# Kernel optimization log

Measured on AMD Instinct MI355X. Metric: run time of the kernel, lower is better.

Reference implementation:

```python
import jax, jax.numpy as jnp
import numpy as np

EPS = 1e-5
K = 16  # neighbors

def bn(x, g, b):
    # BatchNorm in training mode: stats over all axes except the last (channel)
    ax = tuple(range(x.ndim - 1))
    m = x.mean(ax, keepdims=True)
    v = x.var(ax, keepdims=True)
    return g * (x - m) * jax.lax.rsqrt(v + EPS) + b

def setup_inputs() -> dict:
    key = jax.random.key(0)
    ks = jax.random.split(key, 12)
    B, N, M, C, D = 2, 16384, 4096, 32, 64
    H = D // 2
    p = lambda k, s: jax.random.normal(k, s, dtype=jnp.float32) * 0.1
    inp = {}
    inp["xyz"] = jax.random.normal(ks[0], (B, N, 3), dtype=jnp.float32)
    inp["feats"] = jax.random.normal(ks[1], (B, C, N), dtype=jnp.float32)
    inp["sample_idx"] = jax.random.randint(ks[2], (B, M), 0, N, dtype=jnp.int32)
    # RelativePosEncoder mlp: Conv2d(10, H, 1) + BN
    inp["W_pos"] = p(ks[3], (10, H)); inp["b_pos"] = jnp.zeros(H); inp["g_pos"] = jnp.ones(H); inp["be_pos"] = jnp.zeros(H)
    # feature_mlp: Conv2d(C, H, 1) + BN
    inp["W_feat"] = p(ks[4], (C, H)); inp["b_feat"] = jnp.zeros(H); inp["g_feat"] = jnp.ones(H); inp["be_feat"] = jnp.zeros(H)
    # attention score mlp: Conv2d(D, D, 1, bias=False)
    inp["W_score"] = p(ks[5], (D, D))
    # out_mlp: Conv1d(D, D, 1, bias=False) + BN
    inp["W_out"] = p(ks[6], (D, D)); inp["g_out"] = jnp.ones(D); inp["be_out"] = jnp.zeros(D)
    # LFA shortcut: Conv1d(C, D, 1, bias=False) + BN
    inp["W_sc1"] = p(ks[7], (C, D)); inp["g_sc1"] = jnp.ones(D); inp["be_sc1"] = jnp.zeros(D)
    # unit shortcut: Conv1d(C, D, 1, bias=False) + BN
    inp["W_sc2"] = p(ks[8], (C, D)); inp["g_sc2"] = jnp.ones(D); inp["be_sc2"] = jnp.zeros(D)
    return inp

def reference(xyz, feats, sample_idx,
              W_pos, b_pos, g_pos, be_pos,
              W_feat, b_feat, g_feat, be_feat,
              W_score,
              W_out, g_out, be_out,
              W_sc1, g_sc1, be_sc1,
              W_sc2, g_sc2, be_sc2):
    B, C, N = feats.shape
    featsT = jnp.transpose(feats, (0, 2, 1))                    # [B,N,C]
    xyz_ds = jnp.take_along_axis(xyz, sample_idx[:, :, None], axis=1)  # [B,M,3]
    # KNN: squared distances are monotone in cdist -> same topk indices
    d2 = jnp.sum((xyz_ds[:, :, None, :] - xyz[:, None, :, :]) ** 2, axis=-1)  # [B,M,N]
    _, knn_idx = jax.lax.top_k(-d2, K)                           # [B,M,K]
    gather = jax.vmap(lambda pts, idx: pts[idx])
    neigh_xyz = gather(xyz, knn_idx)                             # [B,M,K,3]
    neigh_feats = gather(featsT, knn_idx)                        # [B,M,K,C]
    center_feats = jnp.take_along_axis(featsT, sample_idx[:, :, None], axis=1)  # [B,M,C]
    # relative position encoding
    center = jnp.broadcast_to(xyz_ds[:, :, None, :], neigh_xyz.shape)
    rel = xyz_ds[:, :, None, :] - neigh_xyz                      # [B,M,K,3]
    dist = jnp.linalg.norm(rel, axis=-1, keepdims=True)          # [B,M,K,1]
    posf = jnp.concatenate([center, neigh_xyz, rel, dist], axis=-1)  # [B,M,K,10]
    pos_feats = jax.nn.relu(bn(posf @ W_pos + b_pos, g_pos, be_pos))       # [B,M,K,H]
    feat_feats = jax.nn.relu(bn(neigh_feats @ W_feat + b_feat, g_feat, be_feat))  # [B,M,K,H]
    combined = jnp.concatenate([feat_feats, pos_feats], axis=-1)  # [B,M,K,D]
    # attention pooling: softmax over the K (neighbor) axis
    scores = jax.nn.softmax(combined @ W_score, axis=2)
    pooled = jnp.sum(scores * combined, axis=2)                  # [B,M,D]
    out = jax.nn.relu(bn(pooled @ W_out, g_out, be_out))         # [B,M,D]
    sc1 = bn(jnp.mean(neigh_feats, axis=2) @ W_sc1, g_sc1, be_sc1)
    f_lfa = out + sc1
    f_sc = bn(center_feats @ W_sc2, g_sc2, be_sc2)
    y = jax.nn.relu(f_lfa + f_sc)                                # [B,M,D]
    return xyz_ds, jnp.transpose(y, (0, 2, 1)), sample_idx
```

## Files before the change

kernel.cpp:

```cpp
#include <hip/hip_runtime.h>
#include <math.h>

#define BB 2
#define NN 16384
#define MM 4096
#define C_IN 32
#define D_DIM 64
#define H_DIM 32
#define KNB 16
#define EPSV 1e-5f
#define FLT_BIG 3.0e38f
#define CAPK 128
#define NSPL 4
#define SPTS (NN / NSPL)

#define SPOS_SUM 0
#define SPOS_SQ 32
#define SFEAT_SUM 64
#define SFEAT_SQ 96
#define SSC1_SUM 128
#define SSC1_SQ 192
#define SSC2_SUM 256
#define SSC2_SQ 320
#define SOUT_SUM 384
#define SOUT_SQ 448
#define STATS_LEN 512
#define PA_W 384
#define PB_W 128
#define NBLK (BB * MM / 4)

__device__ __forceinline__ int clampi_r17(int v, int lo, int hi) {
    return v < lo ? lo : (v > hi ? hi : v);
}

__global__ __launch_bounds__(256) void prep_r17(const float* __restrict__ feats,
                                                const float* __restrict__ xyz,
                                                const int* __restrict__ sample_idx,
                                                float* __restrict__ featsT,
                                                float* __restrict__ xyz4,
                                                float* __restrict__ stats,
                                                float* __restrict__ out) {
    __shared__ float tile[C_IN][65];
    const int tid = threadIdx.x;
    const int b = blockIdx.x >> 8;
    const int n0 = (blockIdx.x & 255) * 64;
#pragma unroll
    for (int it = 0; it < 8; ++it) {
        int c = (tid >> 6) + 4 * it;
        int n = tid & 63;
        tile[c][n] = feats[((size_t)b * C_IN + c) * NN + n0 + n];
    }
    int e = blockIdx.x * 256 + tid;
    if (e < STATS_LEN) stats[e] = 0.f;
    if (e < BB * NN) {
        float x = xyz[e * 3 + 0], y = xyz[e * 3 + 1], z = xyz[e * 3 + 2];
        xyz4[e * 4 + 0] = x;
        xyz4[e * 4 + 1] = y;
        xyz4[e * 4 + 2] = z;
        xyz4[e * 4 + 3] = x * x + y * y + z * z;
    }
    if (e < BB * MM) {
        int bb2 = e >> 12;
        int sidx = clampi_r17(sample_idx[e], 0, NN - 1);
        const float* p = xyz + (size_t)(bb2 * NN + sidx) * 3;
        out[e * 3 + 0] = p[0];
        out[e * 3 + 1] = p[1];
        out[e * 3 + 2] = p[2];
        out[BB * MM * 3 + BB * D_DIM * MM + e] = (float)sample_idx[e];
    }
    __syncthreads();
#pragma unroll
    for (int it = 0; it < 8; ++it) {
        int c = tid & 31;
        int nn = (tid >> 5) + 8 * it;
        featsT[((size_t)b * NN + n0 + nn) * C_IN + c] = tile[c][nn];
    }
}

__device__ void knn_fullsplit_r17(const float* __restrict__ base4, int n0,
                                  float m2x, float m2y, float m2z, int lane,
                                  float* __restrict__ outd, int* __restrict__ outi) {
    float d2v[KNB]; int iv[KNB];
#pragma unroll
    for (int i = 0; i < KNB; i++) { d2v[i] = FLT_BIG; iv[i] = 0x7FFFFFFF; }
    float curmax = FLT_BIG; int amax = 0;
    for (int t = 0; t < SPTS / 64; ++t) {
        int n = n0 + lane + t * 64;
        const float4 p = *reinterpret_cast<const float4*>(base4 + (size_t)n * 4);
        float d2 = fmaf(p.x, m2x, p.w);
        d2 = fmaf(p.y, m2y, d2);
        d2 = fmaf(p.z, m2z, d2);
        if (d2 < curmax) {
#pragma unroll
            for (int i = 0; i < KNB; i++)
                if (i == amax) { d2v[i] = d2; iv[i] = n; }
            curmax = d2v[0]; amax = 0;
#pragma unroll
            for (int i = 1; i < KNB; i++)
                if (d2v[i] > curmax) { curmax = d2v[i]; amax = i; }
        }
    }
#pragma unroll
    for (int i = 0; i < KNB; i++) {
#pragma unroll
        for (int j = 0; j < KNB - 1; j++) {
            bool sw = (d2v[j] > d2v[j + 1]) ||
                      (d2v[j] == d2v[j + 1] && iv[j] > iv[j + 1]);
            if (sw) {
                float td = d2v[j]; d2v[j] = d2v[j + 1]; d2v[j + 1] = td;
                int   ti = iv[j];  iv[j]  = iv[j + 1];  iv[j + 1]  = ti;
            }
        }
    }
    float myd = FLT_BIG; int myidx = 0x7FFFFFFF;
#pragma unroll 1
    for (int r = 0; r < KNB; r++) {
        float cv = d2v[0]; int cid = iv[0]; int ml = lane;
#pragma unroll
        for (int off = 32; off > 0; off >>= 1) {
            float ov = __shfl_xor(cv, off);
            int   oid = __shfl_xor(cid, off);
            int   ol = __shfl_xor(ml, off);
            bool take = (ov < cv) || (ov == cv && oid < cid);
            cv = take ? ov : cv; cid = take ? oid : cid; ml = take ? ol : ml;
        }
        if (lane == r) { myd = cv; myidx = cid; }
        if (lane == ml) {
#pragma unroll
            for (int i = 0; i < KNB - 1; i++) { d2v[i] = d2v[i + 1]; iv[i] = iv[i + 1]; }
            d2v[KNB - 1] = FLT_BIG; iv[KNB - 1] = 0x7FFFFFFF;
        }
    }
    if (lane < KNB) { outd[lane] = myd; outi[lane] = myidx; }
}

__global__ __launch_bounds__(256) void knn_r17(const float* __restrict__ xyz4,
                                               const int* __restrict__ sample_idx,
                                               float* __restrict__ cand_d,
                                               int* __restrict__ cand_i) {
    __shared__ float bufd[16][CAPK];
    __shared__ int   bufi[16][CAPK];
    __shared__ int   cnt_lds[16];
    const int tid = threadIdx.x;
    const int w = tid >> 6, lane = tid & 63;
    const int split = blockIdx.x & (NSPL - 1);
    const int qgrp = blockIdx.x >> 2;
    const int qbase = qgrp * 16 + w * 4;
    const int b = qbase >> 12;
    const int n0 = split * SPTS;
    if (tid < 16) cnt_lds[tid] = 0;
    __syncthreads();
    const float* base4 = xyz4 + (size_t)b * NN * 4;
    const float4* p4 = reinterpret_cast<const float4*>(base4) + n0 + lane;

    float m2x[4], m2y[4], m2z[4], md[4], v16[4];
#pragma unroll
    for (int j = 0; j < 4; j++) {
        int s = clampi_r17(sample_idx[qbase + j], 0, NN - 1);
        m2x[j] = -2.f * base4[(size_t)s * 4 + 0];
        m2y[j] = -2.f * base4[(size_t)s * 4 + 1];
        m2z[j] = -2.f * base4[(size_t)s * 4 + 2];
        md[j] = FLT_BIG;
    }
#pragma unroll 8
    for (int it = 0; it < SPTS / 64; ++it) {
        const float4 p = p4[(size_t)it * 64];
#pragma unroll
        for (int j = 0; j < 4; j++) {
            float t = fmaf(p.x, m2x[j], p.w);
            t = fmaf(p.y, m2y[j], t);
            t = fmaf(p.z, m2z[j], t);
            md[j] = fminf(md[j], t);
        }
    }
#pragma unroll 1
    for (int j = 0; j < 4; j++) {
        unsigned fb = __float_as_uint(md[j]);
        unsigned key = (fb & 0x80000000u) ? ~fb : (fb | 0x80000000u);
        unsigned lo = 0u, hi = 0xFFFFFFFFu;
#pragma unroll 1
        for (int itb = 0; itb < 18; ++itb) {
            unsigned mid = lo + ((hi - lo) >> 1);
            unsigned long long bal = __ballot(key <= mid);
            int c = __popcll(bal);
            if (c >= KNB) hi = mid; else lo = mid + 1;
        }
        unsigned vb = (hi & 0x80000000u) ? (hi & 0x7FFFFFFFu) : ~hi;
        v16[j] = __uint_as_float(vb);
    }
#pragma unroll 4
    for (int it = 0; it < SPTS / 64; ++it) {
        const float4 p = p4[(size_t)it * 64];
        const int n = n0 + lane + it * 64;
#pragma unroll
        for (int j = 0; j < 4; j++) {
            float t = fmaf(p.x, m2x[j], p.w);
            t = fmaf(p.y, m2y[j], t);
            t = fmaf(p.z, m2z[j], t);
            if (t <= v16[j]) {
                int pos = atomicAdd(&cnt_lds[w * 4 + j], 1);
                if (pos < CAPK) { bufd[w * 4 + j][pos] = t; bufi[w * 4 + j][pos] = n; }
            }
        }
    }
    __threadfence_block();
#pragma unroll 1
    for (int j = 0; j < 4; j++) {
        const int qi = w * 4 + j;
        const int cnt = cnt_lds[qi];
        const int q = qbase + j;
        float* outd = cand_d + ((size_t)q * NSPL + split) * KNB;
        int*   outi = cand_i + ((size_t)q * NSPL + split) * KNB;
        if (cnt <= CAPK) {
#pragma unroll 1
            for (int half = 0; half < 2; ++half) {
                int i = lane + 64 * half;
                if (i < cnt) {
                    float di = bufd[qi][i]; int xi = bufi[qi][i];
                    int rank = 0;
                    for (int t = 0; t < cnt; ++t) {
                        float dt = bufd[qi][t]; int xt = bufi[qi][t];
                        rank += (dt < di || (dt == di && xt < xi)) ? 1 : 0;
                    }
                    if (rank < KNB) { outd[rank] = di; outi[rank] = xi; }
                }
            }
        } else {
            knn_fullsplit_r17(base4, n0, m2x[j], m2y[j], m2z[j], lane, outd, outi);
        }
    }
}

__device__ __forceinline__ void prebn_r17(const float (*posf)[12], const float (*nf)[C_IN],
                                          int k, int h,
                                          const float* __restrict__ W_pos, const float* __restrict__ b_pos,
                                          const float* __restrict__ W_feat, const float* __restrict__ b_feat,
                                          float* a_out, float* f_out) {
    float4 p0 = *reinterpret_cast<const float4*>(&posf[k][0]);
    float4 p1 = *reinterpret_cast<const float4*>(&posf[k][4]);
    float p8 = posf[k][8], p9 = posf[k][9];
    float a = b_pos[h];
    a += p0.x * W_pos[0 * H_DIM + h]; a += p0.y * W_pos[1 * H_DIM + h];
    a += p0.z * W_pos[2 * H_DIM + h]; a += p0.w * W_pos[3 * H_DIM + h];
    a += p1.x * W_pos[4 * H_DIM + h]; a += p1.y * W_pos[5 * H_DIM + h];
    a += p1.z * W_pos[6 * H_DIM + h]; a += p1.w * W_pos[7 * H_DIM + h];
    a += p8 * W_pos[8 * H_DIM + h];   a += p9 * W_pos[9 * H_DIM + h];
    float f = b_feat[h];
#pragma unroll
    for (int j4 = 0; j4 < C_IN / 4; ++j4) {
        float4 c = *reinterpret_cast<const float4*>(&nf[k][j4 * 4]);
        f += c.x * W_feat[(j4 * 4 + 0) * H_DIM + h];
        f += c.y * W_feat[(j4 * 4 + 1) * H_DIM + h];
        f += c.z * W_feat[(j4 * 4 + 2) * H_DIM + h];
        f += c.w * W_feat[(j4 * 4 + 3) * H_DIM + h];
    }
    *a_out = a; *f_out = f;
}

__global__ __launch_bounds__(256) void stageA_r17(const float* __restrict__ xyz4,
                                                  const int* __restrict__ sample_idx,
                                                  const float* __restrict__ featsT,
                                                  const float* __restrict__ cand_d,
                                                  const int* __restrict__ cand_i,
                                                  const float* __restrict__ W_pos, const float* __restrict__ b_pos,
                                                  const float* __restrict__ W_feat, const float* __restrict__ b_feat,
                                                  const float* __restrict__ W_sc1, const float* __restrict__ W_sc2,
                                                  float* __restrict__ combpre,
                                                  float* __restrict__ sc1_pre, float* __restrict__ sc2_pre,
                                                  float* __restrict__ partialsA) {
    __shared__ int   idxs[4][KNB];
    __shared__ float sd[4][64];
    __shared__ int   si[4][64];
    __shared__ __align__(16) float posf[4][KNB][12];
    __shared__ __align__(16) float nf[4][KNB][C_IN];
    __shared__ float meanf[4][C_IN];
    __shared__ float centerf[4][C_IN];
    __shared__ float posS[4][H_DIM], posQ[4][H_DIM], featS[4][H_DIM], featQ[4][H_DIM];
    __shared__ float s1S[4][D_DIM], s1Q[4][D_DIM], s2S[4][D_DIM], s2Q[4][D_DIM];
    const int tid = threadIdx.x;
    const int w = tid >> 6, lane = tid & 63;
    const int q = blockIdx.x * 4 + w;
    const int b = q >> 12;
    const int sidx = clampi_r17(sample_idx[q], 0, NN - 1);
    const float* base4 = xyz4 + (size_t)b * NN * 4;

    float d = cand_d[(size_t)q * 64 + lane];
    int   i = cand_i[(size_t)q * 64 + lane];
    float qx = base4[(size_t)sidx * 4 + 0];
    float qy = base4[(size_t)sidx * 4 + 1];
    float qz = base4[(size_t)sidx * 4 + 2];
    float cfv = 0.f;
    if (lane < C_IN) cfv = featsT[((size_t)b * NN + sidx) * C_IN + lane];

    {
        sd[w][lane] = d; si[w][lane] = i;
        __syncthreads();
        int rank = 0;
#pragma unroll
        for (int t = 0; t < 64; ++t) {
            float dt = sd[w][t]; int it = si[w][t];
            rank += (dt < d || (dt == d && it < i)) ? 1 : 0;
        }
        if (rank < KNB) idxs[w][rank] = i;
        if (lane < C_IN) centerf[w][lane] = cfv;
        __syncthreads();
    }

    if (lane < KNB) {
        int idx = clampi_r17(idxs[w][lane], 0, NN - 1);
        float nx = base4[(size_t)idx * 4 + 0];
        float ny = base4[(size_t)idx * 4 + 1];
        float nz = base4[(size_t)idx * 4 + 2];
        float rx = qx - nx, ry = qy - ny, rz = qz - nz;
        float dist = sqrtf(rx * rx + ry * ry + rz * rz);
        posf[w][lane][0] = qx; posf[w][lane][1] = qy; posf[w][lane][2] = qz;
        posf[w][lane][3] = nx; posf[w][lane][4] = ny; posf[w][lane][5] = nz;
        posf[w][lane][6] = rx; posf[w][lane][7] = ry; posf[w][lane][8] = rz;
        posf[w][lane][9] = dist; posf[w][lane][10] = 0.f; posf[w][lane][11] = 0.f;
    }
    __syncthreads();
    const float* fT = featsT + (size_t)b * NN * C_IN;
#pragma unroll
    for (int ii = 0; ii < 2; ++ii) {
        int e4 = lane + 64 * ii;
        int k = e4 >> 3, c4 = e4 & 7;
        const float4 v = *reinterpret_cast<const float4*>(fT + (size_t)idxs[w][k] * C_IN + c4 * 4);
        *reinterpret_cast<float4*>(&nf[w][k][c4 * 4]) = v;
    }
    __syncthreads();

    const int h = lane & 31;
    float sP = 0.f, qP = 0.f, sF = 0.f, qF = 0.f;
    float* cp = combpre + (size_t)q * (KNB * D_DIM);
#pragma unroll
    for (int i2 = 0; i2 < 8; i2++) {
        int k = ((lane + 64 * i2) >> 5);
        float a, f;
        prebn_r17(posf[w], nf[w], k, h, W_pos, b_pos, W_feat, b_feat, &a, &f);
        sP += a; qP += a * a;
        sF += f; qF += f * f;
        cp[k * D_DIM + h] = f;
        cp[k * D_DIM + H_DIM + h] = a;
    }
    sP += __shfl_xor(sP, 32); qP += __shfl_xor(qP, 32);
    sF += __shfl_xor(sF, 32); qF += __shfl_xor(qF, 32);
    if (lane < H_DIM) {
        posS[w][h] = sP; posQ[w][h] = qP; featS[w][h] = sF; featQ[w][h] = qF;
    }
    if (lane < C_IN) {
        float s = 0.f;
#pragma unroll
        for (int k = 0; k < KNB; k++) s += nf[w][k][lane];
        meanf[w][lane] = s * (1.f / (float)KNB);
    }
    __syncthreads();
    {
        float a = 0.f, c2 = 0.f;
#pragma unroll
        for (int j = 0; j < C_IN; j++) {
            a  += meanf[w][j]   * W_sc1[j * D_DIM + lane];
            c2 += centerf[w][j] * W_sc2[j * D_DIM + lane];
        }
        sc1_pre[(size_t)q * D_DIM + lane] = a;
        sc2_pre[(size_t)q * D_DIM + lane] = c2;
        s1S[w][lane] = a;  s1Q[w][lane] = a * a;
        s2S[w][lane] = c2; s2Q[w][lane] = c2 * c2;
    }
    __syncthreads();
    float* row = partialsA + (size_t)blockIdx.x * PA_W;
    if (tid < H_DIM) {
        row[SPOS_SUM + tid]  = posS[0][tid] + posS[1][tid] + posS[2][tid] + posS[3][tid];
        row[SPOS_SQ + tid]   = posQ[0][tid] + posQ[1][tid] + posQ[2][tid] + posQ[3][tid];
        row[SFEAT_SUM + tid] = featS[0][tid] + featS[1][tid] + featS[2][tid] + featS[3][tid];
        row[SFEAT_SQ + tid]  = featQ[0][tid] + featQ[1][tid] + featQ[2][tid] + featQ[3][tid];
    } else if (tid >= 64 && tid < 128) {
        int dd = tid - 64;
        row[SSC1_SUM + dd] = s1S[0][dd] + s1S[1][dd] + s1S[2][dd] + s1S[3][dd];
        row[SSC1_SQ + dd]  = s1Q[0][dd] + s1Q[1][dd] + s1Q[2][dd] + s1Q[3][dd];
    } else if (tid >= 128 && tid < 192) {
        int dd = tid - 128;
        row[SSC2_SUM + dd] = s2S[0][dd] + s2S[1][dd] + s2S[2][dd] + s2S[3][dd];
        row[SSC2_SQ + dd]  = s2Q[0][dd] + s2Q[1][dd] + s2Q[2][dd] + s2Q[3][dd];
    }
}

#define NRSPLIT 64
__global__ __launch_bounds__(256) void reduce_r17(const float* __restrict__ partials,
                                                  int rows, int width,
                                                  float* __restrict__ stats_out) {
    const int wchunks = (width + 255) / 256;
    const int wi = blockIdx.x % wchunks;
    const int pi = blockIdx.x / wchunks;
    const int c = wi * 256 + threadIdx.x;
    if (c >= width) return;
    const int per = rows / NRSPLIT;
    const int p0 = pi * per;
    float s = 0.f;
    for (int p = p0; p < p0 + per; ++p) s += partials[(size_t)p * width + c];
    atomicAdd(&stats_out[c], s);
}

__global__ __launch_bounds__(256) void stageB_r17(const float* __restrict__ combpre,
                                                  const float* __restrict__ g_pos, const float* __restrict__ be_pos,
                                                  const float* __restrict__ g_feat, const float* __restrict__ be_feat,
                                                  const float* __restrict__ W_score, const float* __restrict__ W_out,
                                                  const float* __restrict__ stats,
                                                  float* __restrict__ out_pre,
                                                  float* __restrict__ partialsB) {
    __shared__ __align__(16) float comb[4][KNB][D_DIM];
    __shared__ float scl[D_DIM], shf[D_DIM];
    __shared__ float pooled[4][D_DIM];
    __shared__ float oS[4][D_DIM], oQ[4][D_DIM];
    const int tid = threadIdx.x;
    const int w = tid >> 6, lane = tid & 63;
    const int q = blockIdx.x * 4 + w;

    if (tid < D_DIM) {
        const float inv1 = 1.f / (float)(BB * MM * KNB);
        float mean, var, g, bb;
        if (tid < H_DIM) {
            mean = stats[SFEAT_SUM + tid] * inv1;
            var  = fmaxf(stats[SFEAT_SQ + tid] * inv1 - mean * mean, 0.f);
            g = g_feat[tid]; bb = be_feat[tid];
        } else {
            int h = tid - H_DIM;
            mean = stats[SPOS_SUM + h] * inv1;
            var  = fmaxf(stats[SPOS_SQ + h] * inv1 - mean * mean, 0.f);
            g = g_pos[h]; bb = be_pos[h];
        }
        float s = g * rsqrtf(var + EPSV);
        scl[tid] = s;
        shf[tid] = bb - mean * s;
    }
    __syncthreads();

    const float4* src = reinterpret_cast<const float4*>(combpre + (size_t)blockIdx.x * 4 * KNB * D_DIM);
#pragma unroll
    for (int i = 0; i < 4; ++i) {
        int f = tid + 256 * i;
        int qloc = f >> 8;
        int k = (f >> 4) & 15;
        int j4 = f & 15;
        float4 v = src[f];
        int j = j4 * 4;
        v.x = fmaxf(v.x * scl[j + 0] + shf[j + 0], 0.f);
        v.y = fmaxf(v.y * scl[j + 1] + shf[j + 1], 0.f);
        v.z = fmaxf(v.z * scl[j + 2] + shf[j + 2], 0.f);
        v.w = fmaxf(v.w * scl[j + 3] + shf[j + 3], 0.f);
        *reinterpret_cast<float4*>(&comb[qloc][k][j]) = v;
    }
    __syncthreads();

    const int d = lane;
    float s[KNB];
#pragma unroll
    for (int k = 0; k < KNB; k++) s[k] = 0.f;
#pragma unroll 4
    for (int j4 = 0; j4 < D_DIM / 4; ++j4) {
        float w0 = W_score[(j4 * 4 + 0) * D_DIM + d];
        float w1 = W_score[(j4 * 4 + 1) * D_DIM + d];
        float w2 = W_score[(j4 * 4 + 2) * D_DIM + d];
        float w3 = W_score[(j4 * 4 + 3) * D_DIM + d];
#pragma unroll
        for (int k = 0; k < KNB; k++) {
            float4 cb = *reinterpret_cast<const float4*>(&comb[w][k][j4 * 4]);
            s[k] += cb.x * w0 + cb.y * w1 + cb.z * w2 + cb.w * w3;
        }
    }
    float mx = s[0];
#pragma unroll
    for (int k = 1; k < KNB; k++) mx = fmaxf(mx, s[k]);
    float sum = 0.f;
#pragma unroll
    for (int k = 0; k < KNB; k++) { s[k] = __expf(s[k] - mx); sum += s[k]; }
    float inv = 1.f / sum;
    float pv = 0.f;
#pragma unroll
    for (int k = 0; k < KNB; k++) pv += s[k] * inv * comb[w][k][d];
    pooled[w][d] = pv;
    __syncthreads();
    float o = 0.f;
#pragma unroll
    for (int dd = 0; dd < D_DIM; dd++) o += pooled[w][dd] * W_out[dd * D_DIM + d];
    out_pre[(size_t)q * D_DIM + d] = o;
    oS[w][d] = o; oQ[w][d] = o * o;
    __syncthreads();
    float* row = partialsB + (size_t)blockIdx.x * PB_W;
    if (tid < D_DIM) {
        row[tid] = oS[0][tid] + oS[1][tid] + oS[2][tid] + oS[3][tid];
    } else if (tid < 2 * D_DIM) {
        int dd = tid - D_DIM;
        row[D_DIM + dd] = oQ[0][dd] + oQ[1][dd] + oQ[2][dd] + oQ[3][dd];
    }
}

__global__ __launch_bounds__(256) void final_r17(const float* __restrict__ out_pre,
                                                 const float* __restrict__ sc1_pre,
                                                 const float* __restrict__ sc2_pre,
                                                 const float* __restrict__ stats,
                                                 const float* __restrict__ g_out, const float* __restrict__ be_out,
                                                 const float* __restrict__ g_sc1, const float* __restrict__ be_sc1,
                                                 const float* __restrict__ g_sc2, const float* __restrict__ be_sc2,
                                                 float* __restrict__ out) {
    __shared__ float yt[64][65];
    const int tid = threadIdx.x;
    const int blk = blockIdx.x;
    const int b = blk >> 6;
    const int m0 = (blk & 63) * 64;
    const int d = tid & 63;

    const float invn = 1.f / (float)(BB * MM);
    float mo = stats[SOUT_SUM + d] * invn;
    float vo = fmaxf(stats[SOUT_SQ + d] * invn - mo * mo, 0.f);
    float so = g_out[d] * rsqrtf(vo + EPSV);
    float oo = be_out[d] - mo * so;
    float m1 = stats[SSC1_SUM + d] * invn;
    float v1 = fmaxf(stats[SSC1_SQ + d] * invn - m1 * m1, 0.f);
    float s1 = g_sc1[d] * rsqrtf(v1 + EPSV);
    float o1 = be_sc1[d] - m1 * s1;
    float m2 = stats[SSC2_SUM + d] * invn;
    float v2 = fmaxf(stats[SSC2_SQ + d] * invn - m2 * m2, 0.f);
    float s2 = g_sc2[d] * rsqrtf(v2 + EPSV);
    float o2 = be_sc2[d] - m2 * s2;

#pragma unroll
    for (int p = 0; p < 16; p++) {
        int ml = (tid >> 6) + 4 * p;
        size_t q = (size_t)b * MM + m0 + ml;
        float x_out = fmaxf(out_pre[q * D_DIM + d] * so + oo, 0.f);
        float x1 = sc1_pre[q * D_DIM + d] * s1 + o1;
        float x2 = sc2_pre[q * D_DIM + d] * s2 + o2;
        yt[ml][d] = fmaxf(x_out + x1 + x2, 0.f);
    }
    __syncthreads();
#pragma unroll
    for (int p = 0; p < 16; p++) {
        int dr = (tid >> 6) + 4 * p;
        int mc = tid & 63;
        out[BB * MM * 3 + (size_t)b * (D_DIM * MM) + (size_t)dr * MM + m0 + mc] = yt[mc][dr];
    }
}

extern "C" void kernel_launch(void* const* d_in, const int* in_sizes, int n_in,
                              void* d_out, int out_size, void* d_ws, size_t ws_size,
                              hipStream_t stream) {
    const float* xyz        = (const float*)d_in[0];
    const float* feats      = (const float*)d_in[1];
    const int*   sample_idx = (const int*)d_in[2];
    const float* W_pos  = (const float*)d_in[3];
    const float* b_pos  = (const float*)d_in[4];
    const float* g_pos  = (const float*)d_in[5];
    const float* be_pos = (const float*)d_in[6];
    const float* W_feat  = (const float*)d_in[7];
    const float* b_feat  = (const float*)d_in[8];
    const float* g_feat  = (const float*)d_in[9];
    const float* be_feat = (const float*)d_in[10];
    const float* W_score = (const float*)d_in[11];
    const float* W_out  = (const float*)d_in[12];
    const float* g_out  = (const float*)d_in[13];
    const float* be_out = (const float*)d_in[14];
    const float* W_sc1  = (const float*)d_in[15];
    const float* g_sc1  = (const float*)d_in[16];
    const float* be_sc1 = (const float*)d_in[17];
    const float* W_sc2  = (const float*)d_in[18];
    const float* g_sc2  = (const float*)d_in[19];
    const float* be_sc2 = (const float*)d_in[20];

    float* out = (float*)d_out;
    float* ws = (float*)d_ws;

    float* featsT    = ws;
    float* xyz4      = featsT + 1048576;
    float* sc1_pre   = xyz4 + 131072;
    float* sc2_pre   = sc1_pre + 524288;
    float* out_pre   = sc2_pre + 524288;
    float* stats     = out_pre + 524288;
    float* partialsA = stats + STATS_LEN;
    float* partialsB = partialsA + NBLK * PA_W;
    float* cand_d    = partialsB + NBLK * PB_W;
    int*   cand_i    = (int*)(cand_d + (size_t)BB * MM * NSPL * KNB);
    float* combpre   = (float*)(cand_i + (size_t)BB * MM * NSPL * KNB);

    prep_r17<<<BB * (NN / 64), 256, 0, stream>>>(feats, xyz, sample_idx,
                                                 featsT, xyz4, stats, out);

    knn_r17<<<(BB * MM / 16) * NSPL, 256, 0, stream>>>(xyz4, sample_idx, cand_d, cand_i);

    stageA_r17<<<NBLK, 256, 0, stream>>>(xyz4, sample_idx, featsT, cand_d, cand_i,
                                         W_pos, b_pos, W_feat, b_feat, W_sc1, W_sc2,
                                         combpre, sc1_pre, sc2_pre, partialsA);
    reduce_r17<<<2 * NRSPLIT, 256, 0, stream>>>(partialsA, NBLK, PA_W, stats);

    stageB_r17<<<NBLK, 256, 0, stream>>>(combpre,
                                         g_pos, be_pos, g_feat, be_feat,
                                         W_score, W_out, stats, out_pre, partialsB);
    reduce_r17<<<1 * NRSPLIT, 256, 0, stream>>>(partialsB, NBLK, PB_W, stats + SOUT_SUM);

    final_r17<<<BB * (MM / 64), 256, 0, stream>>>(out_pre, sc1_pre, sc2_pre, stats,
                                                  g_out, be_out, g_sc1, be_sc1, g_sc2, be_sc2, out);
}
```

Measured before the change: 260.4 us.

## Use wavefront bitonic sort for KNN candidates and interleave threshold searches

In the KNN kernel, candidate lists of up to 64 entries are now sorted with a register bitonic network using cross-lane shuffles, run for all four queries at once. This replaces the O(cnt^2) rank-counting loop over shared memory, which is kept only as a fallback for larger counts. The four per-query binary searches for the 16th-smallest threshold are interleaved so their ballots can overlap. The block-wide barrier after zeroing the counters becomes per-wave initialization, which relies on each wave touching only its own counters.

```diff
diff --git a/kernel.cpp b/kernel.cpp
--- a/kernel.cpp
+++ b/kernel.cpp
@@ -29,11 +29,11 @@
 #define PB_W 128
 #define NBLK (BB * MM / 4)
 
-__device__ __forceinline__ int clampi_r17(int v, int lo, int hi) {
+__device__ __forceinline__ int clampi_r18(int v, int lo, int hi) {
     return v < lo ? lo : (v > hi ? hi : v);
 }
 
-__global__ __launch_bounds__(256) void prep_r17(const float* __restrict__ feats,
+__global__ __launch_bounds__(256) void prep_r18(const float* __restrict__ feats,
                                                 const float* __restrict__ xyz,
                                                 const int* __restrict__ sample_idx,
                                                 float* __restrict__ featsT,
@@ -61,7 +61,7 @@
     }
     if (e < BB * MM) {
         int bb2 = e >> 12;
-        int sidx = clampi_r17(sample_idx[e], 0, NN - 1);
+        int sidx = clampi_r18(sample_idx[e], 0, NN - 1);
         const float* p = xyz + (size_t)(bb2 * NN + sidx) * 3;
         out[e * 3 + 0] = p[0];
         out[e * 3 + 1] = p[1];
@@ -77,7 +77,7 @@
     }
 }
 
-__device__ void knn_fullsplit_r17(const float* __restrict__ base4, int n0,
+__device__ void knn_fullsplit_r18(const float* __restrict__ base4, int n0,
                                   float m2x, float m2y, float m2z, int lane,
                                   float* __restrict__ outd, int* __restrict__ outi) {
     float d2v[KNB]; int iv[KNB];
@@ -134,7 +134,7 @@
     if (lane < KNB) { outd[lane] = myd; outi[lane] = myidx; }
 }
 
-__global__ __launch_bounds__(256) void knn_r17(const float* __restrict__ xyz4,
+__global__ __launch_bounds__(256) void knn_r18(const float* __restrict__ xyz4,
                                                const int* __restrict__ sample_idx,
                                                float* __restrict__ cand_d,
                                                int* __restrict__ cand_i) {
@@ -148,15 +148,14 @@
     const int qbase = qgrp * 16 + w * 4;
     const int b = qbase >> 12;
     const int n0 = split * SPTS;
-    if (tid < 16) cnt_lds[tid] = 0;
-    __syncthreads();
+    if (lane < 4) cnt_lds[w * 4 + lane] = 0;
     const float* base4 = xyz4 + (size_t)b * NN * 4;
     const float4* p4 = reinterpret_cast<const float4*>(base4) + n0 + lane;
 
     float m2x[4], m2y[4], m2z[4], md[4], v16[4];
 #pragma unroll
     for (int j = 0; j < 4; j++) {
-        int s = clampi_r17(sample_idx[qbase + j], 0, NN - 1);
+        int s = clampi_r18(sample_idx[qbase + j], 0, NN - 1);
         m2x[j] = -2.f * base4[(size_t)s * 4 + 0];
         m2y[j] = -2.f * base4[(size_t)s * 4 + 1];
         m2z[j] = -2.f * base4[(size_t)s * 4 + 2];
@@ -173,20 +172,29 @@
             md[j] = fminf(md[j], t);
         }
     }
-#pragma unroll 1
-    for (int j = 0; j < 4; j++) {
-        unsigned fb = __float_as_uint(md[j]);
-        unsigned key = (fb & 0x80000000u) ? ~fb : (fb | 0x80000000u);
-        unsigned lo = 0u, hi = 0xFFFFFFFFu;
+    {
+        unsigned key[4], lo[4], hi[4];
+#pragma unroll
+        for (int j = 0; j < 4; j++) {
+            unsigned fb = __float_as_uint(md[j]);
+            key[j] = (fb & 0x80000000u) ? ~fb : (fb | 0x80000000u);
+            lo[j] = 0u; hi[j] = 0xFFFFFFFFu;
+        }
 #pragma unroll 1
         for (int itb = 0; itb < 18; ++itb) {
-            unsigned mid = lo + ((hi - lo) >> 1);
-            unsigned long long bal = __ballot(key <= mid);
-            int c = __popcll(bal);
-            if (c >= KNB) hi = mid; else lo = mid + 1;
-        }
-        unsigned vb = (hi & 0x80000000u) ? (hi & 0x7FFFFFFFu) : ~hi;
-        v16[j] = __uint_as_float(vb);
+#pragma unroll
+            for (int j = 0; j < 4; j++) {
+                unsigned mid = lo[j] + ((hi[j] - lo[j]) >> 1);
+                unsigned long long bal = __ballot(key[j] <= mid);
+                int c = __popcll(bal);
+                if (c >= KNB) hi[j] = mid; else lo[j] = mid + 1;
+            }
+        }
+#pragma unroll
+        for (int j = 0; j < 4; j++) {
+            unsigned vb = (hi[j] & 0x80000000u) ? (hi[j] & 0x7FFFFFFFu) : ~hi[j];
+            v16[j] = __uint_as_float(vb);
+        }
     }
 #pragma unroll 4
     for (int it = 0; it < SPTS / 64; ++it) {
@@ -204,34 +212,66 @@
         }
     }
     __threadfence_block();
-#pragma unroll 1
-    for (int j = 0; j < 4; j++) {
-        const int qi = w * 4 + j;
-        const int cnt = cnt_lds[qi];
-        const int q = qbase + j;
-        float* outd = cand_d + ((size_t)q * NSPL + split) * KNB;
-        int*   outi = cand_i + ((size_t)q * NSPL + split) * KNB;
-        if (cnt <= CAPK) {
-#pragma unroll 1
-            for (int half = 0; half < 2; ++half) {
-                int i = lane + 64 * half;
-                if (i < cnt) {
-                    float di = bufd[qi][i]; int xi = bufi[qi][i];
-                    int rank = 0;
-                    for (int t = 0; t < cnt; ++t) {
-                        float dt = bufd[qi][t]; int xt = bufi[qi][t];
-                        rank += (dt < di || (dt == di && xt < xi)) ? 1 : 0;
-                    }
-                    if (rank < KNB) { outd[rank] = di; outi[rank] = xi; }
+    {
+        float dv[4]; int ivv[4]; int cnts[4];
+#pragma unroll
+        for (int j = 0; j < 4; j++) {
+            const int qi = w * 4 + j;
+            int cnt = cnt_lds[qi];
+            cnts[j] = cnt;
+            bool valid = (cnt <= 64) && (lane < cnt);
+            dv[j]  = valid ? bufd[qi][lane] : FLT_BIG;
+            ivv[j] = valid ? bufi[qi][lane] : 0x7FFFFFFF;
+        }
+#pragma unroll
+        for (int k = 2; k <= 64; k <<= 1) {
+#pragma unroll
+            for (int j2 = k >> 1; j2 >= 1; j2 >>= 1) {
+                const bool lower = ((lane & j2) == 0);
+                const bool dirup = ((lane & k) == 0);
+                const bool want_min = (lower == dirup);
+#pragma unroll
+                for (int j = 0; j < 4; j++) {
+                    float od = __shfl_xor(dv[j], j2);
+                    int   oi = __shfl_xor(ivv[j], j2);
+                    bool mine_less = (dv[j] < od) || (dv[j] == od && ivv[j] < oi);
+                    bool keep = (mine_less == want_min);
+                    dv[j]  = keep ? dv[j]  : od;
+                    ivv[j] = keep ? ivv[j] : oi;
                 }
             }
-        } else {
-            knn_fullsplit_r17(base4, n0, m2x[j], m2y[j], m2z[j], lane, outd, outi);
-        }
-    }
-}
-
-__device__ __forceinline__ void prebn_r17(const float (*posf)[12], const float (*nf)[C_IN],
+        }
+#pragma unroll 1
+        for (int j = 0; j < 4; j++) {
+            const int qi = w * 4 + j;
+            const int cnt = cnts[j];
+            const int q = qbase + j;
+            float* outd = cand_d + ((size_t)q * NSPL + split) * KNB;
+            int*   outi = cand_i + ((size_t)q * NSPL + split) * KNB;
+            if (cnt <= 64) {
+                if (lane < KNB) { outd[lane] = dv[j]; outi[lane] = ivv[j]; }
+            } else if (cnt <= CAPK) {
+#pragma unroll 1
+                for (int half = 0; half < 2; ++half) {
+                    int i = lane + 64 * half;
+                    if (i < cnt) {
+                        float di = bufd[qi][i]; int xi = bufi[qi][i];
+                        int rank = 0;
+                        for (int t = 0; t < cnt; ++t) {
+                            float dt = bufd[qi][t]; int xt = bufi[qi][t];
+                            rank += (dt < di || (dt == di && xt < xi)) ? 1 : 0;
+                        }
+                        if (rank < KNB) { outd[rank] = di; outi[rank] = xi; }
+                    }
+                }
+            } else {
+                knn_fullsplit_r18(base4, n0, m2x[j], m2y[j], m2z[j], lane, outd, outi);
+            }
+        }
+    }
+}
+
+__device__ __forceinline__ void prebn_r18(const float (*posf)[12], const float (*nf)[C_IN],
                                           int k, int h,
                                           const float* __restrict__ W_pos, const float* __restrict__ b_pos,
                                           const float* __restrict__ W_feat, const float* __restrict__ b_feat,
@@ -257,7 +297,7 @@
     *a_out = a; *f_out = f;
 }
 
-__global__ __launch_bounds__(256) void stageA_r17(const float* __restrict__ xyz4,
+__global__ __launch_bounds__(256) void stageA_r18(const float* __restrict__ xyz4,
                                                   const int* __restrict__ sample_idx,
                                                   const float* __restrict__ featsT,
                                                   const float* __restrict__ cand_d,
@@ -281,7 +321,7 @@
     const int w = tid >> 6, lane = tid & 63;
     const int q = blockIdx.x * 4 + w;
     const int b = q >> 12;
-    const int sidx = clampi_r17(sample_idx[q], 0, NN - 1);
+    const int sidx = clampi_r18(sample_idx[q], 0, NN - 1);
     const float* base4 = xyz4 + (size_t)b * NN * 4;
 
     float d = cand_d[(size_t)q * 64 + lane];
@@ -307,7 +347,7 @@
     }
 
     if (lane < KNB) {
-        int idx = clampi_r17(idxs[w][lane], 0, NN - 1);
+        int idx = clampi_r18(idxs[w][lane], 0, NN - 1);
         float nx = base4[(size_t)idx * 4 + 0];
         float ny = base4[(size_t)idx * 4 + 1];
         float nz = base4[(size_t)idx * 4 + 2];
@@ -336,7 +376,7 @@
     for (int i2 = 0; i2 < 8; i2++) {
         int k = ((lane + 64 * i2) >> 5);
         float a, f;
-        prebn_r17(posf[w], nf[w], k, h, W_pos, b_pos, W_feat, b_feat, &a, &f);
+        prebn_r18(posf[w], nf[w], k, h, W_pos, b_pos, W_feat, b_feat, &a, &f);
         sP += a; qP += a * a;
         sF += f; qF += f * f;
         cp[k * D_DIM + h] = f;
@@ -385,7 +425,7 @@
 }
 
 #define NRSPLIT 64
-__global__ __launch_bounds__(256) void reduce_r17(const float* __restrict__ partials,
+__global__ __launch_bounds__(256) void reduce_r18(const float* __restrict__ partials,
                                                   int rows, int width,
                                                   float* __restrict__ stats_out) {
     const int wchunks = (width + 255) / 256;
@@ -400,7 +440,7 @@
     atomicAdd(&stats_out[c], s);
 }
 
-__global__ __launch_bounds__(256) void stageB_r17(const float* __restrict__ combpre,
+__global__ __launch_bounds__(256) void stageB_r18(const float* __restrict__ combpre,
                                                   const float* __restrict__ g_pos, const float* __restrict__ be_pos,
                                                   const float* __restrict__ g_feat, const float* __restrict__ be_feat,
                                                   const float* __restrict__ W_score, const float* __restrict__ W_out,
@@ -494,7 +534,7 @@
     }
 }
 
-__global__ __launch_bounds__(256) void final_r17(const float* __restrict__ out_pre,
+__global__ __launch_bounds__(256) void final_r18(const float* __restrict__ out_pre,
                                                  const float* __restrict__ sc1_pre,
                                                  const float* __restrict__ sc2_pre,
                                                  const float* __restrict__ stats,
@@ -581,21 +621,21 @@
     int*   cand_i    = (int*)(cand_d + (size_t)BB * MM * NSPL * KNB);
     float* combpre   = (float*)(cand_i + (size_t)BB * MM * NSPL * KNB);
 
-    prep_r17<<<BB * (NN / 64), 256, 0, stream>>>(feats, xyz, sample_idx,
+    prep_r18<<<BB * (NN / 64), 256, 0, stream>>>(feats, xyz, sample_idx,
                                                  featsT, xyz4, stats, out);
 
-    knn_r17<<<(BB * MM / 16) * NSPL, 256, 0, stream>>>(xyz4, sample_idx, cand_d, cand_i);
-
-    stageA_r17<<<NBLK, 256, 0, stream>>>(xyz4, sample_idx, featsT, cand_d, cand_i,
+    knn_r18<<<(BB * MM / 16) * NSPL, 256, 0, stream>>>(xyz4, sample_idx, cand_d, cand_i);
+
+    stageA_r18<<<NBLK, 256, 0, stream>>>(xyz4, sample_idx, featsT, cand_d, cand_i,
                                          W_pos, b_pos, W_feat, b_feat, W_sc1, W_sc2,
                                          combpre, sc1_pre, sc2_pre, partialsA);
-    reduce_r17<<<2 * NRSPLIT, 256, 0, stream>>>(partialsA, NBLK, PA_W, stats);
-
-    stageB_r17<<<NBLK, 256, 0, stream>>>(combpre,
+    reduce_r18<<<2 * NRSPLIT, 256, 0, stream>>>(partialsA, NBLK, PA_W, stats);
+
+    stageB_r18<<<NBLK, 256, 0, stream>>>(combpre,
                                          g_pos, be_pos, g_feat, be_feat,
                                          W_score, W_out, stats, out_pre, partialsB);
-    reduce_r17<<<1 * NRSPLIT, 256, 0, stream>>>(partialsB, NBLK, PB_W, stats + SOUT_SUM);
-
-    final_r17<<<BB * (MM / 64), 256, 0, stream>>>(out_pre, sc1_pre, sc2_pre, stats,
+    reduce_r18<<<1 * NRSPLIT, 256, 0, stream>>>(partialsB, NBLK, PB_W, stats + SOUT_SUM);
+
+    final_r18<<<BB * (MM / 64), 256, 0, stream>>>(out_pre, sc1_pre, sc2_pre, stats,
                                                   g_out, be_out, g_sc1, be_sc1, g_sc2, be_sc2, out);
 }
```

New measurement: 254.3 us. -2.4%, faster.
